# Kernel tuning notes

Measured on AMD Instinct MI355X. Metric: run time of the kernel, lower is better.

## Reference

```python
import jax, jax.numpy as jnp
import numpy as np

G = 128          # resolution
NE = 4           # n_emotions
SIGMA = 0.05     # splat kernel width
ETA = 0.01       # global write strength
ALPHA_H = 0.002
ALPHA_E = 0.001
LEAK = 5e-05
RADIUS = max(2, int(3.0 * SIGMA * G / 2.0))   # = 9
W = 2 * RADIUS + 1                            # = 19


def _laplacian(x):
    # 6-neighbor Laplacian with replicate padding; x: [..., G, G, G]
    pad = [(0, 0)] * (x.ndim - 3) + [(1, 1)] * 3
    p = jnp.pad(x, pad, mode='edge')
    c = p[..., 1:-1, 1:-1, 1:-1]
    return (p[..., :-2, 1:-1, 1:-1] + p[..., 2:, 1:-1, 1:-1]
            + p[..., 1:-1, :-2, 1:-1] + p[..., 1:-1, 2:, 1:-1]
            + p[..., 1:-1, 1:-1, :-2] + p[..., 1:-1, 1:-1, 2:]
            - 6.0 * c)


def _splat(H, E, positions, intensities, emotions):
    # Gaussian splat scatter-add into H [G,G,G] and E [NE,G,G,G].
    gp = (positions + 1.0) * 0.5 * (G - 1)                       # [N,3] grid coords
    c = jnp.clip(jnp.floor(gp).astype(jnp.int32), 0, G - 1)      # center cell
    offs = jnp.arange(-RADIUS, RADIUS + 1, dtype=jnp.int32)
    coords = c[:, :, None] + offs[None, None, :]                 # [N,3,W]
    valid = (coords >= 0) & (coords < G)
    cc = jnp.clip(coords, 0, G - 1)
    sig = SIGMA * G / 2.0
    d = coords.astype(gp.dtype) - gp[:, :, None]                 # [N,3,W]
    k1 = jnp.where(valid, jnp.exp(-(d * d) / (2.0 * sig * sig)), 0.0)
    kx, ky, kz = k1[:, 0], k1[:, 1], k1[:, 2]                    # [N,W] each (separable)
    omega = intensities * ETA                                    # [N]
    vals = (omega[:, None, None, None] * kx[:, :, None, None]
            * ky[:, None, :, None] * kz[:, None, None, :])       # [N,W,W,W]
    flat = ((cc[:, 0][:, :, None, None] * G + cc[:, 1][:, None, :, None]) * G
            + cc[:, 2][:, None, None, :]).reshape(-1)            # [N*W^3]
    H_new = H.reshape(-1).at[flat].add(vals.reshape(-1)).reshape(G, G, G)
    E_ch = []
    for e in range(NE):
        ve = (vals * emotions[:, e][:, None, None, None]).reshape(-1)
        E_ch.append(E[e].reshape(-1).at[flat].add(ve).reshape(G, G, G))
    return H_new, jnp.stack(E_ch)


def _step(H, E):
    H2 = jnp.maximum(H * (1.0 - LEAK) + ALPHA_H * _laplacian(H), 0.0)
    E2 = jnp.maximum(E * (1.0 - LEAK) + LEAK + ALPHA_E * _laplacian(E), 0.0)
    return H2, E2


def _sample(H, E, sp):
    # grid_sample trilinear, padding_mode='border', align_corners=True.
    # grid_sample axis convention: sp[...,0]->last axis, sp[...,1]->middle, sp[...,2]->first.
    B, T, _ = sp.shape
    t = jnp.clip((sp.reshape(-1, 3) + 1.0) * 0.5 * (G - 1), 0.0, G - 1)  # [BT,3]
    i0 = jnp.floor(t).astype(jnp.int32)
    f = t - i0
    i0 = jnp.clip(i0, 0, G - 1)
    i1 = jnp.clip(i0 + 1, 0, G - 1)
    x0, y0, z0 = i0[:, 0], i0[:, 1], i0[:, 2]
    x1, y1, z1 = i1[:, 0], i1[:, 1], i1[:, 2]
    fx, fy, fz = f[:, 0], f[:, 1], f[:, 2]

    def interp(vol):  # vol [..., G,G,G] -> [..., BT]
        out = 0.0
        for zi, wz in ((z0, 1.0 - fz), (z1, fz)):
            for yi, wy in ((y0, 1.0 - fy), (y1, fy)):
                for xi, wx in ((x0, 1.0 - fx), (x1, fx)):
                    out = out + vol[..., zi, yi, xi] * (wz * wy * wx)
        return out

    p_H = interp(H).reshape(B, T)
    p_E = interp(E).T.reshape(B, T, NE)
    return p_H, p_E


def setup_inputs() -> dict:
    key = jax.random.key(0)
    k1, k2, k3, k4 = jax.random.split(key, 4)
    N, B, T = 4096, 8, 1024
    return {
        'positions': jax.random.uniform(k1, (N, 3), jnp.float32, -0.95, 0.95),
        'intensities': jax.random.uniform(k2, (N,), jnp.float32),
        'emotions': jax.random.uniform(k3, (N, NE), jnp.float32),
        'sample_positions': jax.random.uniform(k4, (B, T, 3), jnp.float32, -1.0, 1.0),
        'H0': jnp.zeros((G, G, G), jnp.float32),
        'E0': jnp.ones((NE, G, G, G), jnp.float32),
    }


def reference(positions, intensities, emotions, sample_positions, H0, E0):
    H, E = _splat(H0, E0, positions, intensities, emotions)
    H, E = _step(H, E)
    p_H, p_E = _sample(H, E, sample_positions)
    return jnp.concatenate([p_H[..., None], p_E], axis=-1)  # [B,T,1+NE]
```

## Files before the change

kernel.cpp:

```cpp
#include <hip/hip_runtime.h>


namespace {
constexpr int   G      = 128;
constexpr int   G3     = G * G * G;
constexpr int   NE     = 4;
constexpr int   RAD    = 9;
constexpr float SIG    = 0.05f * (float)G * 0.5f;
constexpr float INV2S2 = 1.0f / (2.0f * SIG * SIG);
constexpr float ETA    = 0.01f;
constexpr float A_H    = 0.002f;
constexpr float A_E    = 0.001f;
constexpr float LEAK   = 5e-5f;

constexpr int T0 = 8, T1 = 4, T2 = 16;
constexpr int NT0 = G / T0, NT1 = G / T1, NT2 = G / T2;
constexpr int NTILES = NT0 * NT1 * NT2;
constexpr int CAP  = 88;
constexpr int PSTR = 32;
constexpr int CSTR = 32;
}

__device__ __forceinline__ int clampi(int v, int lo, int hi) {
    return min(max(v, lo), hi);
}

__global__ void __launch_bounds__(256) bin_meta_kernel(
        const float* __restrict__ pos, const float* __restrict__ inten,
        const float4* __restrict__ emo4,
        int* __restrict__ counts, int* __restrict__ lists,
        float4* __restrict__ meta, int N) {
    const int p    = blockIdx.x * 4 + (threadIdx.x >> 6);
    const int lane = threadIdx.x & 63;
    if (p >= N) return;

    const float gx = (pos[p * 3 + 0] + 1.0f) * 0.5f * (float)(G - 1);
    const float gy = (pos[p * 3 + 1] + 1.0f) * 0.5f * (float)(G - 1);
    const float gz = (pos[p * 3 + 2] + 1.0f) * 0.5f * (float)(G - 1);
    const int c0 = clampi((int)floorf(gx), 0, G - 1);
    const int c1 = clampi((int)floorf(gy), 0, G - 1);
    const int c2 = clampi((int)floorf(gz), 0, G - 1);

    if (lane == 0) {
        meta[2 * p]     = make_float4(gx, gy, gz, inten[p] * ETA);
        meta[2 * p + 1] = emo4[p];
    }

    const int l0 = max(c0 - RAD, 0) >> 3, h0 = min(c0 + RAD, G - 1) >> 3;
    const int l1 = max(c1 - RAD, 0) >> 2, h1 = min(c1 + RAD, G - 1) >> 2;
    const int l2 = max(c2 - RAD, 0) >> 4, h2 = min(c2 + RAD, G - 1) >> 4;
    const int n0 = h0 - l0, n1 = h1 - l1, n2 = h2 - l2;

    for (int s = lane; s < 72; s += 64) {
        const int a  = s / 18;
        const int r  = s - a * 18;
        const int b  = r / 3;
        const int cs = r - b * 3;
        if (a <= n0 && b <= n1 && cs <= n2) {
            const int t = ((l0 + a) * NT1 + (l1 + b)) * NT2 + (l2 + cs);
            const int slot = atomicAdd(&counts[t * CSTR], 1);
            if (slot < CAP) lists[t * CAP + slot] = p;
        }
    }
}

__global__ void __launch_bounds__(128) gather_kernel(
        const float4* __restrict__ meta,
        const float* __restrict__ H0, const float* __restrict__ E0,
        const int* __restrict__ counts, const int* __restrict__ lists,
        float* __restrict__ ws) {
    const int tile = blockIdx.x;
    const int t2 = tile & (NT2 - 1);
    const int t1 = (tile >> 3) & (NT1 - 1);
    const int t0 = tile >> 8;
    const int tid = threadIdx.x;

    __shared__ __align__(16) float tab[CAP * PSTR];

    const int cnt = min(counts[tile * CSTR], CAP);
    const int* __restrict__ lst = lists + tile * CAP;
    const int b0 = t0 * T0, b1 = t1 * T1, b2 = t2 * T2;

    for (int t = tid; t < cnt * PSTR; t += 128) {
        const int n = t >> 5;
        const int s = t & 31;
        const int p = lst[n];
        float v;
        if (s >= 8 && s < 12) {
            const float4 me = meta[2 * p + 1];
            const int q = s - 8;
            v = (q == 0) ? me.x : (q == 1) ? me.y : (q == 2) ? me.z : me.w;
        } else {
            const float4 mg = meta[2 * p];
            float g; int base, off;
            if (s < 8)       { g = mg.x; base = b0; off = s;      }
            else if (s < 16) { g = mg.y; base = b1; off = s - 12; }
            else             { g = mg.z; base = b2; off = s - 16; }
            const int cc = clampi((int)floorf(g), 0, G - 1);
            const int coord = base + off;
            const float d = (float)coord - g;
            v = (abs(coord - cc) <= RAD) ? __expf(-d * d * INV2S2) : 0.0f;
            if (s < 8) v *= mg.w;
        }
        tab[n * PSTR + s] = v;
    }
    __syncthreads();

    const int k  = tid & (T2 - 1);
    const int j  = (tid >> 4) & (T1 - 1);
    const int i4 = (tid >> 6) * 4;

    const int x2 = b2 + k, x1 = b1 + j;
    const int flat0 = ((b0 + i4) * G + x1) * G + x2;

    float h[4], e[NE][4];
#pragma unroll
    for (int i = 0; i < 4; ++i) {
        h[i] = H0[flat0 + i * G * G];
#pragma unroll
        for (int c = 0; c < NE; ++c) e[c][i] = E0[c * G3 + flat0 + i * G * G];
    }

    const float* __restrict__ tkx = tab + i4;
    const float* __restrict__ tky = tab + 12 + j;
    const float* __restrict__ tkz = tab + 16 + k;

    for (int n = 0; n < cnt; ++n) {
        const float4 kxv = *(const float4*)(tkx + n * PSTR);
        const float4 emv = *(const float4*)(tab + n * PSTR + 8);
        const float  kyz = tky[n * PSTR] * tkz[n * PSTR];
        const float w0 = kxv.x * kyz, w1 = kxv.y * kyz,
                    w2 = kxv.z * kyz, w3 = kxv.w * kyz;
        h[0] += w0;  h[1] += w1;  h[2] += w2;  h[3] += w3;
        e[0][0] += w0 * emv.x; e[0][1] += w1 * emv.x;
        e[0][2] += w2 * emv.x; e[0][3] += w3 * emv.x;
        e[1][0] += w0 * emv.y; e[1][1] += w1 * emv.y;
        e[1][2] += w2 * emv.y; e[1][3] += w3 * emv.y;
        e[2][0] += w0 * emv.z; e[2][1] += w1 * emv.z;
        e[2][2] += w2 * emv.z; e[2][3] += w3 * emv.z;
        e[3][0] += w0 * emv.w; e[3][1] += w1 * emv.w;
        e[3][2] += w2 * emv.w; e[3][3] += w3 * emv.w;
    }

#pragma unroll
    for (int i = 0; i < 4; ++i) {
        ws[flat0 + i * G * G] = h[i];
#pragma unroll
        for (int c = 0; c < NE; ++c)
            ws[(c + 1) * G3 + flat0 + i * G * G] = e[c][i];
    }
}

__device__ __forceinline__ float stepped_at(const float* __restrict__ vol,
                                            int z, int y, int x,
                                            float addc, float alpha) {
    const int zm = max(z - 1, 0), zp = min(z + 1, G - 1);
    const int ym = max(y - 1, 0), yp = min(y + 1, G - 1);
    const int xm = max(x - 1, 0), xp = min(x + 1, G - 1);
    const float cv  = vol[(z * G + y) * G + x];
    const float lap = vol[(zm * G + y) * G + x] + vol[(zp * G + y) * G + x]
                    + vol[(z * G + ym) * G + x] + vol[(z * G + yp) * G + x]
                    + vol[(z * G + y) * G + xm] + vol[(z * G + y) * G + xp]
                    - 6.0f * cv;
    const float s = cv * (1.0f - LEAK) + addc + alpha * lap;
    return fmaxf(s, 0.0f);
}

__global__ void __launch_bounds__(256) sample_kernel(
        const float* __restrict__ sp, const float* __restrict__ ws,
        float* __restrict__ out, int n_out) {
    const int gt = blockIdx.x * blockDim.x + threadIdx.x;
    const int corner = gt & 7;
    const int o = gt >> 3;
    if (o >= n_out) return;
    const int c = o % 5;
    const int p = o / 5;

    const float t0 = fminf(fmaxf((sp[p * 3 + 0] + 1.0f) * 0.5f * (float)(G - 1), 0.0f), (float)(G - 1));
    const float t1 = fminf(fmaxf((sp[p * 3 + 1] + 1.0f) * 0.5f * (float)(G - 1), 0.0f), (float)(G - 1));
    const float t2 = fminf(fmaxf((sp[p * 3 + 2] + 1.0f) * 0.5f * (float)(G - 1), 0.0f), (float)(G - 1));

    const int a0 = (int)floorf(t0);  const float f0 = t0 - (float)a0;
    const int a1 = (int)floorf(t1);  const float f1 = t1 - (float)a1;
    const int a2 = (int)floorf(t2);  const float f2 = t2 - (float)a2;
    const int b0 = min(a0 + 1, G - 1);
    const int b1 = min(a1 + 1, G - 1);
    const int b2 = min(a2 + 1, G - 1);

    const int d0 = corner & 1, d1 = (corner >> 1) & 1, d2 = corner >> 2;
    const int   x = d0 ? b0 : a0;
    const int   y = d1 ? b1 : a1;
    const int   z = d2 ? b2 : a2;
    const float w = (d0 ? f0 : 1.0f - f0) * (d1 ? f1 : 1.0f - f1)
                  * (d2 ? f2 : 1.0f - f2);

    const float* vol  = ws + (size_t)c * G3;
    const float addc  = (c == 0) ? 0.0f : LEAK;
    const float alpha = (c == 0) ? A_H : A_E;

    float v = w * stepped_at(vol, z, y, x, addc, alpha);
    v += __shfl_xor(v, 1);
    v += __shfl_xor(v, 2);
    v += __shfl_xor(v, 4);
    if (corner == 0) out[o] = v;
}

extern "C" void kernel_launch(void* const* d_in, const int* in_sizes, int n_in,
                              void* d_out, int out_size, void* d_ws, size_t ws_size,
                              hipStream_t stream) {
    const float* positions   = (const float*)d_in[0];
    const float* intensities = (const float*)d_in[1];
    const float* emotions    = (const float*)d_in[2];
    const float* sample_pos  = (const float*)d_in[3];
    const float* H0          = (const float*)d_in[4];
    const float* E0          = (const float*)d_in[5];
    float* ws  = (float*)d_ws;
    float* out = (float*)d_out;

    const int N = in_sizes[0] / 3;

    int*    counts = (int*)(ws + 5 * (size_t)G3);
    int*    lists  = counts + (size_t)NTILES * CSTR;
    float4* meta   = (float4*)(lists + (size_t)NTILES * CAP);

    hipMemsetAsync(counts, 0, (size_t)NTILES * CSTR * sizeof(int), stream);

    bin_meta_kernel<<<(N + 3) / 4, 256, 0, stream>>>(
        positions, intensities, (const float4*)emotions, counts, lists, meta, N);

    gather_kernel<<<NTILES, 128, 0, stream>>>(
        meta, H0, E0, counts, lists, ws);

    const int n_thr = out_size * 8;
    sample_kernel<<<(n_thr + 255) / 256, 256, 0, stream>>>(
        sample_pos, ws, out, out_size);
}
```

Baseline: 137.4 us.

## Evaluate splat and diffusion step analytically at sample points instead of materializing grids

Removes the full-volume gather kernel that built five 128^3 grids in workspace. A fused kernel now evaluates the stepped base volumes (H0, E0) only at the trilinear corners of each sample point. It adds the Gaussian splat contribution and its Laplacian per particle using separable 1D kernels and the linearity of the step. Particle binning is widened so each tile's list covers every particle that can reach a sample's corner stencil, and the per-tile capacity is raised. The per-corner ReLU is dropped, which is exact only while the stepped values stay non-negative, and particles beyond the list capacity are still silently dropped.

```diff
diff --git a/kernel.cpp b/kernel.cpp
--- a/kernel.cpp
+++ b/kernel.cpp
@@ -4,7 +4,6 @@
 namespace {
 constexpr int   G      = 128;
 constexpr int   G3     = G * G * G;
-constexpr int   NE     = 4;
 constexpr int   RAD    = 9;
 constexpr float SIG    = 0.05f * (float)G * 0.5f;
 constexpr float INV2S2 = 1.0f / (2.0f * SIG * SIG);
@@ -16,8 +15,7 @@
 constexpr int T0 = 8, T1 = 4, T2 = 16;
 constexpr int NT0 = G / T0, NT1 = G / T1, NT2 = G / T2;
 constexpr int NTILES = NT0 * NT1 * NT2;
-constexpr int CAP  = 88;
-constexpr int PSTR = 32;
+constexpr int CAP  = 96;
 constexpr int CSTR = 32;
 }
 
@@ -46,108 +44,24 @@
         meta[2 * p + 1] = emo4[p];
     }
 
-    const int l0 = max(c0 - RAD, 0) >> 3, h0 = min(c0 + RAD, G - 1) >> 3;
-    const int l1 = max(c1 - RAD, 0) >> 2, h1 = min(c1 + RAD, G - 1) >> 2;
-    const int l2 = max(c2 - RAD, 0) >> 4, h2 = min(c2 + RAD, G - 1) >> 4;
-    const int n0 = h0 - l0, n1 = h1 - l1, n2 = h2 - l2;
-
-    for (int s = lane; s < 72; s += 64) {
-        const int a  = s / 18;
-        const int r  = s - a * 18;
+    const int t0lo = (max(c0 - 18, 0) + T0 - 1) >> 3;
+    const int t0hi = min(c0 + 10, G - 1) >> 3;
+    const int t1lo = (max(c1 - 14, 0) + T1 - 1) >> 2;
+    const int t1hi = min(c1 + 10, G - 1) >> 2;
+    const int t2lo = (max(c2 - 26, 0) + T2 - 1) >> 4;
+    const int t2hi = min(c2 + 10, G - 1) >> 4;
+    const int n0 = t0hi - t0lo, n1 = t1hi - t1lo, n2 = t2hi - t2lo;
+
+    for (int s = lane; s < 84; s += 64) {
+        const int a  = s / 21;
+        const int r  = s - a * 21;
         const int b  = r / 3;
         const int cs = r - b * 3;
         if (a <= n0 && b <= n1 && cs <= n2) {
-            const int t = ((l0 + a) * NT1 + (l1 + b)) * NT2 + (l2 + cs);
+            const int t = ((t0lo + a) * NT1 + (t1lo + b)) * NT2 + (t2lo + cs);
             const int slot = atomicAdd(&counts[t * CSTR], 1);
             if (slot < CAP) lists[t * CAP + slot] = p;
         }
-    }
-}
-
-__global__ void __launch_bounds__(128) gather_kernel(
-        const float4* __restrict__ meta,
-        const float* __restrict__ H0, const float* __restrict__ E0,
-        const int* __restrict__ counts, const int* __restrict__ lists,
-        float* __restrict__ ws) {
-    const int tile = blockIdx.x;
-    const int t2 = tile & (NT2 - 1);
-    const int t1 = (tile >> 3) & (NT1 - 1);
-    const int t0 = tile >> 8;
-    const int tid = threadIdx.x;
-
-    __shared__ __align__(16) float tab[CAP * PSTR];
-
-    const int cnt = min(counts[tile * CSTR], CAP);
-    const int* __restrict__ lst = lists + tile * CAP;
-    const int b0 = t0 * T0, b1 = t1 * T1, b2 = t2 * T2;
-
-    for (int t = tid; t < cnt * PSTR; t += 128) {
-        const int n = t >> 5;
-        const int s = t & 31;
-        const int p = lst[n];
-        float v;
-        if (s >= 8 && s < 12) {
-            const float4 me = meta[2 * p + 1];
-            const int q = s - 8;
-            v = (q == 0) ? me.x : (q == 1) ? me.y : (q == 2) ? me.z : me.w;
-        } else {
-            const float4 mg = meta[2 * p];
-            float g; int base, off;
-            if (s < 8)       { g = mg.x; base = b0; off = s;      }
-            else if (s < 16) { g = mg.y; base = b1; off = s - 12; }
-            else             { g = mg.z; base = b2; off = s - 16; }
-            const int cc = clampi((int)floorf(g), 0, G - 1);
-            const int coord = base + off;
-            const float d = (float)coord - g;
-            v = (abs(coord - cc) <= RAD) ? __expf(-d * d * INV2S2) : 0.0f;
-            if (s < 8) v *= mg.w;
-        }
-        tab[n * PSTR + s] = v;
-    }
-    __syncthreads();
-
-    const int k  = tid & (T2 - 1);
-    const int j  = (tid >> 4) & (T1 - 1);
-    const int i4 = (tid >> 6) * 4;
-
-    const int x2 = b2 + k, x1 = b1 + j;
-    const int flat0 = ((b0 + i4) * G + x1) * G + x2;
-
-    float h[4], e[NE][4];
-#pragma unroll
-    for (int i = 0; i < 4; ++i) {
-        h[i] = H0[flat0 + i * G * G];
-#pragma unroll
-        for (int c = 0; c < NE; ++c) e[c][i] = E0[c * G3 + flat0 + i * G * G];
-    }
-
-    const float* __restrict__ tkx = tab + i4;
-    const float* __restrict__ tky = tab + 12 + j;
-    const float* __restrict__ tkz = tab + 16 + k;
-
-    for (int n = 0; n < cnt; ++n) {
-        const float4 kxv = *(const float4*)(tkx + n * PSTR);
-        const float4 emv = *(const float4*)(tab + n * PSTR + 8);
-        const float  kyz = tky[n * PSTR] * tkz[n * PSTR];
-        const float w0 = kxv.x * kyz, w1 = kxv.y * kyz,
-                    w2 = kxv.z * kyz, w3 = kxv.w * kyz;
-        h[0] += w0;  h[1] += w1;  h[2] += w2;  h[3] += w3;
-        e[0][0] += w0 * emv.x; e[0][1] += w1 * emv.x;
-        e[0][2] += w2 * emv.x; e[0][3] += w3 * emv.x;
-        e[1][0] += w0 * emv.y; e[1][1] += w1 * emv.y;
-        e[1][2] += w2 * emv.y; e[1][3] += w3 * emv.y;
-        e[2][0] += w0 * emv.z; e[2][1] += w1 * emv.z;
-        e[2][2] += w2 * emv.z; e[2][3] += w3 * emv.z;
-        e[3][0] += w0 * emv.w; e[3][1] += w1 * emv.w;
-        e[3][2] += w2 * emv.w; e[3][3] += w3 * emv.w;
-    }
-
-#pragma unroll
-    for (int i = 0; i < 4; ++i) {
-        ws[flat0 + i * G * G] = h[i];
-#pragma unroll
-        for (int c = 0; c < NE; ++c)
-            ws[(c + 1) * G3 + flat0 + i * G * G] = e[c][i];
     }
 }
 
@@ -162,47 +76,105 @@
                     + vol[(z * G + ym) * G + x] + vol[(z * G + yp) * G + x]
                     + vol[(z * G + y) * G + xm] + vol[(z * G + y) * G + xp]
                     - 6.0f * cv;
-    const float s = cv * (1.0f - LEAK) + addc + alpha * lap;
-    return fmaxf(s, 0.0f);
-}
-
-__global__ void __launch_bounds__(256) sample_kernel(
-        const float* __restrict__ sp, const float* __restrict__ ws,
-        float* __restrict__ out, int n_out) {
-    const int gt = blockIdx.x * blockDim.x + threadIdx.x;
-    const int corner = gt & 7;
-    const int o = gt >> 3;
-    if (o >= n_out) return;
-    const int c = o % 5;
-    const int p = o / 5;
-
-    const float t0 = fminf(fmaxf((sp[p * 3 + 0] + 1.0f) * 0.5f * (float)(G - 1), 0.0f), (float)(G - 1));
-    const float t1 = fminf(fmaxf((sp[p * 3 + 1] + 1.0f) * 0.5f * (float)(G - 1), 0.0f), (float)(G - 1));
-    const float t2 = fminf(fmaxf((sp[p * 3 + 2] + 1.0f) * 0.5f * (float)(G - 1), 0.0f), (float)(G - 1));
-
-    const int a0 = (int)floorf(t0);  const float f0 = t0 - (float)a0;
-    const int a1 = (int)floorf(t1);  const float f1 = t1 - (float)a1;
-    const int a2 = (int)floorf(t2);  const float f2 = t2 - (float)a2;
-    const int b0 = min(a0 + 1, G - 1);
-    const int b1 = min(a1 + 1, G - 1);
-    const int b2 = min(a2 + 1, G - 1);
-
-    const int d0 = corner & 1, d1 = (corner >> 1) & 1, d2 = corner >> 2;
-    const int   x = d0 ? b0 : a0;
-    const int   y = d1 ? b1 : a1;
-    const int   z = d2 ? b2 : a2;
-    const float w = (d0 ? f0 : 1.0f - f0) * (d1 ? f1 : 1.0f - f1)
-                  * (d2 ? f2 : 1.0f - f2);
-
-    const float* vol  = ws + (size_t)c * G3;
-    const float addc  = (c == 0) ? 0.0f : LEAK;
-    const float alpha = (c == 0) ? A_H : A_E;
-
-    float v = w * stepped_at(vol, z, y, x, addc, alpha);
-    v += __shfl_xor(v, 1);
-    v += __shfl_xor(v, 2);
-    v += __shfl_xor(v, 4);
-    if (corner == 0) out[o] = v;
+    return cv * (1.0f - LEAK) + addc + alpha * lap;
+}
+
+__device__ __forceinline__ void axis_eval(float g, int ia, int ib,
+        int ma, int pa, int mb, int pb, float wa, float wb,
+        float& dir, float& lap) {
+    const int cp = clampi((int)floorf(g), 0, G - 1);
+    auto kf = [&](int v) -> float {
+        const float d = (float)v - g;
+        const float e = __expf(-d * d * INV2S2);
+        return (abs(v - cp) <= RAD) ? e : 0.0f;
+    };
+    const float ka = kf(ia), kb = kf(ib);
+    lap = wa * (kf(ma) + kf(pa) - 2.0f * ka)
+        + wb * (kf(mb) + kf(pb) - 2.0f * kb);
+    dir = wa * ka + wb * kb;
+}
+
+__global__ void __launch_bounds__(256) fused_sample_kernel(
+        const float* __restrict__ sp, const float4* __restrict__ meta,
+        const int* __restrict__ counts, const int* __restrict__ lists,
+        const float* __restrict__ H0, const float* __restrict__ E0,
+        float* __restrict__ out, int n_samp) {
+    const int wave = (blockIdx.x * blockDim.x + threadIdx.x) >> 6;
+    const int lane = threadIdx.x & 63;
+    if (wave >= n_samp) return;
+
+    const float s0 = sp[wave * 3 + 0];
+    const float s1 = sp[wave * 3 + 1];
+    const float s2 = sp[wave * 3 + 2];
+    const float uz = fminf(fmaxf((s2 + 1.0f) * 0.5f * (float)(G - 1), 0.0f), (float)(G - 1));
+    const float uy = fminf(fmaxf((s1 + 1.0f) * 0.5f * (float)(G - 1), 0.0f), (float)(G - 1));
+    const float ux = fminf(fmaxf((s0 + 1.0f) * 0.5f * (float)(G - 1), 0.0f), (float)(G - 1));
+    const int za = (int)floorf(uz); const float fz = uz - (float)za;
+    const int ya = (int)floorf(uy); const float fy = uy - (float)ya;
+    const int xa = (int)floorf(ux); const float fx = ux - (float)xa;
+    const int zb = min(za + 1, G - 1);
+    const int yb = min(ya + 1, G - 1);
+    const int xb = min(xa + 1, G - 1);
+
+    float bv = 0.0f;
+    if (lane < 40) {
+        const int c = lane >> 3, corner = lane & 7;
+        const int d0 = corner & 1, d1 = (corner >> 1) & 1, d2 = corner >> 2;
+        const int x = d0 ? xb : xa, y = d1 ? yb : ya, z = d2 ? zb : za;
+        const float w = (d0 ? fx : 1.0f - fx) * (d1 ? fy : 1.0f - fy)
+                      * (d2 ? fz : 1.0f - fz);
+        const float* vol  = (c == 0) ? H0 : E0 + (size_t)(c - 1) * G3;
+        const float addc  = (c == 0) ? 0.0f : LEAK;
+        const float alpha = (c == 0) ? A_H : A_E;
+        bv = w * stepped_at(vol, z, y, x, addc, alpha);
+    }
+    bv += __shfl_xor(bv, 1);
+    bv += __shfl_xor(bv, 2);
+    bv += __shfl_xor(bv, 4);
+
+    const int tile = ((za >> 3) * NT1 + (ya >> 2)) * NT2 + (xa >> 4);
+    const int cnt = min(counts[tile * CSTR], CAP);
+    const int* __restrict__ lst = lists + tile * CAP;
+
+    const int zma = max(za - 1, 0), zpa = min(za + 1, G - 1);
+    const int zmb = max(zb - 1, 0), zpb = min(zb + 1, G - 1);
+    const int yma = max(ya - 1, 0), ypa = min(ya + 1, G - 1);
+    const int ymb = max(yb - 1, 0), ypb = min(yb + 1, G - 1);
+    const int xma = max(xa - 1, 0), xpa = min(xa + 1, G - 1);
+    const int xmb = max(xb - 1, 0), xpb = min(xb + 1, G - 1);
+    const float wza = 1.0f - fz, wzb = fz;
+    const float wya = 1.0f - fy, wyb = fy;
+    const float wxa = 1.0f - fx, wxb = fx;
+
+    float aH = 0.0f, aE0 = 0.0f, aE1 = 0.0f, aE2 = 0.0f, aE3 = 0.0f;
+    for (int nb = lane; nb < cnt; nb += 64) {
+        const int p = lst[nb];
+        const float4 mg = meta[2 * p];
+        const float4 me = meta[2 * p + 1];
+        float dz_, lz_, dy_, ly_, dx_, lx_;
+        axis_eval(mg.x, za, zb, zma, zpa, zmb, zpb, wza, wzb, dz_, lz_);
+        axis_eval(mg.y, ya, yb, yma, ypa, ymb, ypb, wya, wyb, dy_, ly_);
+        axis_eval(mg.z, xa, xb, xma, xpa, xmb, xpb, wxa, wxb, dx_, lx_);
+        const float b3 = dz_ * dy_ * dx_;
+        const float l3 = lz_ * dy_ * dx_ + dz_ * ly_ * dx_ + dz_ * dy_ * lx_;
+        const float cH = mg.w * ((1.0f - LEAK) * b3 + A_H * l3);
+        const float cE = mg.w * ((1.0f - LEAK) * b3 + A_E * l3);
+        aH  += cH;
+        aE0 += cE * me.x;  aE1 += cE * me.y;
+        aE2 += cE * me.z;  aE3 += cE * me.w;
+    }
+
+#define RED64(v) { v += __shfl_xor(v, 1);  v += __shfl_xor(v, 2);  \
+                   v += __shfl_xor(v, 4);  v += __shfl_xor(v, 8);  \
+                   v += __shfl_xor(v, 16); v += __shfl_xor(v, 32); }
+    RED64(aH) RED64(aE0) RED64(aE1) RED64(aE2) RED64(aE3)
+#undef RED64
+
+    const int  src   = (lane < 5) ? lane * 8 : 0;
+    const float basec = __shfl(bv, src);
+    const float sv = (lane == 0) ? aH  : (lane == 1) ? aE0
+                   : (lane == 2) ? aE1 : (lane == 3) ? aE2 : aE3;
+    if (lane < 5) out[wave * 5 + lane] = basec + sv;
 }
 
 extern "C" void kernel_launch(void* const* d_in, const int* in_sizes, int n_in,
@@ -214,12 +186,11 @@
     const float* sample_pos  = (const float*)d_in[3];
     const float* H0          = (const float*)d_in[4];
     const float* E0          = (const float*)d_in[5];
-    float* ws  = (float*)d_ws;
     float* out = (float*)d_out;
 
     const int N = in_sizes[0] / 3;
 
-    int*    counts = (int*)(ws + 5 * (size_t)G3);
+    int*    counts = (int*)d_ws;
     int*    lists  = counts + (size_t)NTILES * CSTR;
     float4* meta   = (float4*)(lists + (size_t)NTILES * CAP);
 
@@ -228,10 +199,7 @@
     bin_meta_kernel<<<(N + 3) / 4, 256, 0, stream>>>(
         positions, intensities, (const float4*)emotions, counts, lists, meta, N);
 
-    gather_kernel<<<NTILES, 128, 0, stream>>>(
-        meta, H0, E0, counts, lists, ws);
-
-    const int n_thr = out_size * 8;
-    sample_kernel<<<(n_thr + 255) / 256, 256, 0, stream>>>(
-        sample_pos, ws, out, out_size);
-}
+    const int n_samp = out_size / 5;
+    fused_sample_kernel<<<(n_samp + 3) / 4, 256, 0, stream>>>(
+        sample_pos, meta, counts, lists, H0, E0, out, n_samp);
+}
```

Result: faster. 113.8 us (-17.2%).
